# Kernel optimization log

Hardware: AMD Instinct MI355X
Metric: run time of the kernel (lower is better)

## Reference

```python
import jax, jax.numpy as jnp
import numpy as np

B, N, M, D = 8, 4096, 4096, 2


def setup_inputs() -> dict:
    key = jax.random.key(0)
    k1, k2, k3, k4 = jax.random.split(key, 4)
    return {
        "predicted_coords": jax.random.normal(k1, (B, N, D), dtype=jnp.float32),
        "predicted_points": jax.random.randint(k2, (B,), N // 2, N + 1, dtype=jnp.int32),
        "target_coords": jax.random.normal(k3, (B, M, D), dtype=jnp.float32),
        "target_points": jax.random.randint(k4, (B,), M // 2, M + 1, dtype=jnp.int32),
    }


def reference(predicted_coords, predicted_points, target_coords, target_points):
    # predicted_coords: [B, N, D], target_coords: [B, M, D]
    # predicted_points / target_points: [B] valid counts
    n = predicted_coords.shape[1]
    d = predicted_coords.shape[2]

    # points_loss = MSE(pred_counts/N, target_counts/N) over the batch
    points_loss = jnp.mean(
        (predicted_points.astype(jnp.float32) / n - target_points.astype(jnp.float32) / n) ** 2
    )

    # Batched 1-NN: squared pairwise distances [B, N, M], invalid targets masked to +inf.
    # (argmin of squared Euclidean == argmin of Euclidean, matching KDTree k=1.)
    d2 = jnp.sum((predicted_coords[:, :, None, :] - target_coords[:, None, :, :]) ** 2, axis=-1)
    tmask = jnp.arange(target_coords.shape[1])[None, :] < target_points[:, None]  # [B, M]
    d2 = jnp.where(tmask[:, None, :], d2, jnp.inf)
    idx = jnp.argmin(d2, axis=-1)  # [B, N]

    # Matched targets are detached in the original (numpy round-trip) -> stop_gradient.
    matched = jax.lax.stop_gradient(
        jnp.take_along_axis(target_coords, idx[:, :, None], axis=1)
    )  # [B, N, D]

    sq = jnp.sum((predicted_coords - matched) ** 2, axis=-1)  # [B, N]
    pmask = jnp.arange(predicted_coords.shape[1])[None, :] < predicted_points[:, None]  # [B, N]
    # Per-sample MSE over valid pred points (mean over count*D elements), then mean over batch.
    denom = predicted_points.astype(jnp.float32) * d
    coord_loss = jnp.mean(jnp.sum(jnp.where(pmask, sq, 0.0), axis=-1) / denom)

    total_loss = coord_loss + 0.1 * points_loss
    return (total_loss, coord_loss, points_loss)
```

## Files before the change

kernel.cpp:

```cpp
#include <hip/hip_runtime.h>
#include <math.h>

#define NB 8
#define NPTS 4096
#define MPTS 4096
#define CHUNK 64
#define NCHUNK (NPTS / CHUNK)
#define NWAVE 8
#define TQ (MPTS / NWAVE)

__device__ __forceinline__ float waveReduceSum(float v) {
#pragma unroll
    for (int off = 32; off > 0; off >>= 1)
        v += __shfl_down(v, off, 64);
    return v;
}

__global__ __launch_bounds__(NWAVE * 64) void nn_kernel(
    const float2* __restrict__ pred,
    const int* __restrict__ pcounts,
    const float2* __restrict__ tgt,
    const int* __restrict__ tcounts,
    float* __restrict__ partials)
{
    __shared__ float sx[MPTS];
    __shared__ float sy[MPTS];
    __shared__ float sc[MPTS];
    __shared__ float mnw[NWAVE][CHUNK];

    const int g = blockIdx.x;
    const int b = g >> 6;
    const int c = g & (NCHUNK - 1);
    const int w = threadIdx.x >> 6;
    const int lane = threadIdx.x & 63;

    const int tcount = tcounts[b];
    const int tstart = w * TQ;

    const float2* tsrc = tgt + (size_t)b * MPTS + tstart;
#pragma unroll
    for (int i = 0; i < TQ / 64; ++i) {
        float2 t = tsrc[i * 64 + lane];
        int idx = tstart + i * 64 + lane;
        sx[idx] = -2.0f * t.x;
        sy[idx] = -2.0f * t.y;
        sc[idx] = fmaf(t.x, t.x, t.y * t.y);
    }

    const float2 p = pred[(size_t)b * NPTS + c * CHUNK + lane];

    int tloc = min(tcount - tstart, TQ);
    if (tloc < 0) tloc = 0;

    float m0 = INFINITY, m1 = INFINITY, m2 = INFINITY, m3 = INFINITY;
    const float4* x4 = (const float4*)&sx[tstart];
    const float4* y4 = (const float4*)&sy[tstart];
    const float4* c4 = (const float4*)&sc[tstart];
    const int nt4 = tloc >> 2;
    for (int i = 0; i < nt4; ++i) {
        float4 xv = x4[i], yv = y4[i], cv = c4[i];
        m0 = fminf(m0, fmaf(p.y, yv.x, fmaf(p.x, xv.x, cv.x)));
        m1 = fminf(m1, fmaf(p.y, yv.y, fmaf(p.x, xv.y, cv.y)));
        m2 = fminf(m2, fmaf(p.y, yv.z, fmaf(p.x, xv.z, cv.z)));
        m3 = fminf(m3, fmaf(p.y, yv.w, fmaf(p.x, xv.w, cv.w)));
    }
    for (int m = nt4 * 4; m < tloc; ++m) {
        float v = fmaf(p.y, sy[tstart + m], fmaf(p.x, sx[tstart + m], sc[tstart + m]));
        m0 = fminf(m0, v);
    }
    mnw[w][lane] = fminf(fminf(m0, m1), fminf(m2, m3));
    __syncthreads();

    if (w == 0) {
        float mn = mnw[0][lane];
#pragma unroll
        for (int j = 1; j < NWAVE; ++j) mn = fminf(mn, mnw[j][lane]);
        float pp = fmaf(p.x, p.x, p.y * p.y);
        float v = (c * CHUNK + lane < pcounts[b]) ? (mn + pp) : 0.0f;
        v = waveReduceSum(v);
        if (lane == 0) partials[g] = v;
    }
}

__global__ __launch_bounds__(512) void final_kernel(
    const float* __restrict__ partials,
    const int* __restrict__ pcounts,
    const int* __restrict__ tcounts,
    float* __restrict__ out)
{
    __shared__ float bs[NB];
    const int w = threadIdx.x >> 6;
    const int lane = threadIdx.x & 63;
    float v = partials[w * NCHUNK + lane];
    v = waveReduceSum(v);
    if (lane == 0) bs[w] = v;
    __syncthreads();
    if (threadIdx.x == 0) {
        float coord = 0.0f, pts = 0.0f;
        for (int b = 0; b < NB; ++b) {
            coord += bs[b] / ((float)pcounts[b] * 2.0f);
            float d = ((float)pcounts[b] - (float)tcounts[b]) / (float)NPTS;
            pts += d * d;
        }
        coord *= (1.0f / NB);
        pts *= (1.0f / NB);
        out[0] = coord + 0.1f * pts;
        out[1] = coord;
        out[2] = pts;
    }
}

extern "C" void kernel_launch(void* const* d_in, const int* in_sizes, int n_in,
                              void* d_out, int out_size, void* d_ws, size_t ws_size,
                              hipStream_t stream) {
    const float2* pred    = (const float2*)d_in[0];
    const int*    pcounts = (const int*)d_in[1];
    const float2* tgt     = (const float2*)d_in[2];
    const int*    tcounts = (const int*)d_in[3];
    float* out = (float*)d_out;

    float* partials = (float*)d_ws;

    nn_kernel<<<NB * NCHUNK, NWAVE * 64, 0, stream>>>(
        pred, pcounts, tgt, tcounts, partials);
    final_kernel<<<1, 512, 0, stream>>>(partials, pcounts, tcounts, out);
}
```

Measured before the change: 20.33 us.

## Split target set across blocks with register-blocked preds and separate min-combine kernel

Restructures the nearest-neighbor search so each block handles a 128-target slice for 1024 predictions, with each thread keeping 4 predictions in registers to reuse every shared-memory target load. Partial minima per slice go to a workspace buffer of 32 slices. A new combine kernel takes the min across slices, adds the squared norm, masks invalid predictions and reduces. The aim is less shared-memory load traffic per FMA and no full-target staging per block, at the cost of an extra kernel launch and about 4 MB of global writes and reads for the partial minima.

```diff
diff --git a/kernel.cpp b/kernel.cpp
--- a/kernel.cpp
+++ b/kernel.cpp
@@ -4,10 +4,15 @@
 #define NB 8
 #define NPTS 4096
 #define MPTS 4096
-#define CHUNK 64
-#define NCHUNK (NPTS / CHUNK)
-#define NWAVE 8
-#define TQ (MPTS / NWAVE)
+#define BN (NB * NPTS)
+#define P 4
+#define WV 4
+#define TT 128
+#define NS (MPTS / TT)
+#define PREDS_PER_WAVE (64 * P)
+#define PREDS_PER_BLOCK (PREDS_PER_WAVE * WV)
+#define PGROUPS (BN / PREDS_PER_BLOCK)
+#define NCHUNK 64
 
 __device__ __forceinline__ float waveReduceSum(float v) {
 #pragma unroll
@@ -16,70 +21,99 @@
     return v;
 }
 
-__global__ __launch_bounds__(NWAVE * 64) void nn_kernel(
+__global__ __launch_bounds__(WV * 64) void nn_kernel(
+    const float2* __restrict__ pred,
+    const float2* __restrict__ tgt,
+    const int* __restrict__ tcounts,
+    float* __restrict__ mins)
+{
+    __shared__ float sx[TT];
+    __shared__ float sy[TT];
+    __shared__ float sc[TT];
+    const int bid = blockIdx.x;
+    const int s  = bid & (NS - 1);
+    const int pg = bid >> 5;
+    const int b  = pg >> 2;
+    const int tid = threadIdx.x;
+
+    const int tcount = tcounts[b];
+    const int tstart = s * TT;
+    const int tloc = min(tcount - tstart, TT);
+
+    if (tid < TT) {
+        float2 t = tgt[(size_t)b * MPTS + tstart + tid];
+        sx[tid] = -2.0f * t.x;
+        sy[tid] = -2.0f * t.y;
+        sc[tid] = fmaf(t.x, t.x, t.y * t.y);
+    }
+    __syncthreads();
+
+    const int w = tid >> 6, lane = tid & 63;
+    const size_t pbase = (size_t)pg * PREDS_PER_BLOCK + w * PREDS_PER_WAVE + lane;
+    const float2 p0 = pred[pbase];
+    const float2 p1 = pred[pbase + 64];
+    const float2 p2 = pred[pbase + 128];
+    const float2 p3 = pred[pbase + 192];
+
+    float mn0 = INFINITY, mn1 = INFINITY, mn2 = INFINITY, mn3 = INFINITY;
+
+    if (tloc > 0) {
+        const float4* x4 = (const float4*)sx;
+        const float4* y4 = (const float4*)sy;
+        const float4* c4 = (const float4*)sc;
+        const int nt4 = tloc >> 2;
+#pragma unroll 2
+        for (int i = 0; i < nt4; ++i) {
+            float4 xv = x4[i], yv = y4[i], cv = c4[i];
+            mn0 = fminf(mn0, fmaf(p0.y, yv.x, fmaf(p0.x, xv.x, cv.x)));
+            mn1 = fminf(mn1, fmaf(p1.y, yv.x, fmaf(p1.x, xv.x, cv.x)));
+            mn2 = fminf(mn2, fmaf(p2.y, yv.x, fmaf(p2.x, xv.x, cv.x)));
+            mn3 = fminf(mn3, fmaf(p3.y, yv.x, fmaf(p3.x, xv.x, cv.x)));
+            mn0 = fminf(mn0, fmaf(p0.y, yv.y, fmaf(p0.x, xv.y, cv.y)));
+            mn1 = fminf(mn1, fmaf(p1.y, yv.y, fmaf(p1.x, xv.y, cv.y)));
+            mn2 = fminf(mn2, fmaf(p2.y, yv.y, fmaf(p2.x, xv.y, cv.y)));
+            mn3 = fminf(mn3, fmaf(p3.y, yv.y, fmaf(p3.x, xv.y, cv.y)));
+            mn0 = fminf(mn0, fmaf(p0.y, yv.z, fmaf(p0.x, xv.z, cv.z)));
+            mn1 = fminf(mn1, fmaf(p1.y, yv.z, fmaf(p1.x, xv.z, cv.z)));
+            mn2 = fminf(mn2, fmaf(p2.y, yv.z, fmaf(p2.x, xv.z, cv.z)));
+            mn3 = fminf(mn3, fmaf(p3.y, yv.z, fmaf(p3.x, xv.z, cv.z)));
+            mn0 = fminf(mn0, fmaf(p0.y, yv.w, fmaf(p0.x, xv.w, cv.w)));
+            mn1 = fminf(mn1, fmaf(p1.y, yv.w, fmaf(p1.x, xv.w, cv.w)));
+            mn2 = fminf(mn2, fmaf(p2.y, yv.w, fmaf(p2.x, xv.w, cv.w)));
+            mn3 = fminf(mn3, fmaf(p3.y, yv.w, fmaf(p3.x, xv.w, cv.w)));
+        }
+        for (int m = nt4 * 4; m < tloc; ++m) {
+            float xs = sx[m], ys = sy[m], cs = sc[m];
+            mn0 = fminf(mn0, fmaf(p0.y, ys, fmaf(p0.x, xs, cs)));
+            mn1 = fminf(mn1, fmaf(p1.y, ys, fmaf(p1.x, xs, cs)));
+            mn2 = fminf(mn2, fmaf(p2.y, ys, fmaf(p2.x, xs, cs)));
+            mn3 = fminf(mn3, fmaf(p3.y, ys, fmaf(p3.x, xs, cs)));
+        }
+    }
+    float* dst = mins + (size_t)s * BN + pbase;
+    dst[0]   = mn0;
+    dst[64]  = mn1;
+    dst[128] = mn2;
+    dst[192] = mn3;
+}
+
+__global__ __launch_bounds__(256) void combine_kernel(
+    const float* __restrict__ mins,
     const float2* __restrict__ pred,
     const int* __restrict__ pcounts,
-    const float2* __restrict__ tgt,
-    const int* __restrict__ tcounts,
     float* __restrict__ partials)
 {
-    __shared__ float sx[MPTS];
-    __shared__ float sy[MPTS];
-    __shared__ float sc[MPTS];
-    __shared__ float mnw[NWAVE][CHUNK];
-
-    const int g = blockIdx.x;
-    const int b = g >> 6;
-    const int c = g & (NCHUNK - 1);
-    const int w = threadIdx.x >> 6;
-    const int lane = threadIdx.x & 63;
-
-    const int tcount = tcounts[b];
-    const int tstart = w * TQ;
-
-    const float2* tsrc = tgt + (size_t)b * MPTS + tstart;
+    const int idx = blockIdx.x * 256 + threadIdx.x;
+    const int b = idx >> 12;
+    const int n = idx & (NPTS - 1);
+    float v = mins[idx];
 #pragma unroll
-    for (int i = 0; i < TQ / 64; ++i) {
-        float2 t = tsrc[i * 64 + lane];
-        int idx = tstart + i * 64 + lane;
-        sx[idx] = -2.0f * t.x;
-        sy[idx] = -2.0f * t.y;
-        sc[idx] = fmaf(t.x, t.x, t.y * t.y);
-    }
-
-    const float2 p = pred[(size_t)b * NPTS + c * CHUNK + lane];
-
-    int tloc = min(tcount - tstart, TQ);
-    if (tloc < 0) tloc = 0;
-
-    float m0 = INFINITY, m1 = INFINITY, m2 = INFINITY, m3 = INFINITY;
-    const float4* x4 = (const float4*)&sx[tstart];
-    const float4* y4 = (const float4*)&sy[tstart];
-    const float4* c4 = (const float4*)&sc[tstart];
-    const int nt4 = tloc >> 2;
-    for (int i = 0; i < nt4; ++i) {
-        float4 xv = x4[i], yv = y4[i], cv = c4[i];
-        m0 = fminf(m0, fmaf(p.y, yv.x, fmaf(p.x, xv.x, cv.x)));
-        m1 = fminf(m1, fmaf(p.y, yv.y, fmaf(p.x, xv.y, cv.y)));
-        m2 = fminf(m2, fmaf(p.y, yv.z, fmaf(p.x, xv.z, cv.z)));
-        m3 = fminf(m3, fmaf(p.y, yv.w, fmaf(p.x, xv.w, cv.w)));
-    }
-    for (int m = nt4 * 4; m < tloc; ++m) {
-        float v = fmaf(p.y, sy[tstart + m], fmaf(p.x, sx[tstart + m], sc[tstart + m]));
-        m0 = fminf(m0, v);
-    }
-    mnw[w][lane] = fminf(fminf(m0, m1), fminf(m2, m3));
-    __syncthreads();
-
-    if (w == 0) {
-        float mn = mnw[0][lane];
-#pragma unroll
-        for (int j = 1; j < NWAVE; ++j) mn = fminf(mn, mnw[j][lane]);
-        float pp = fmaf(p.x, p.x, p.y * p.y);
-        float v = (c * CHUNK + lane < pcounts[b]) ? (mn + pp) : 0.0f;
-        v = waveReduceSum(v);
-        if (lane == 0) partials[g] = v;
-    }
+    for (int s = 1; s < NS; ++s) v = fminf(v, mins[(size_t)s * BN + idx]);
+    float2 p = pred[idx];
+    v += fmaf(p.x, p.x, p.y * p.y);
+    v = (n < pcounts[b]) ? v : 0.0f;
+    v = waveReduceSum(v);
+    if ((threadIdx.x & 63) == 0) partials[idx >> 6] = v;
 }
 
 __global__ __launch_bounds__(512) void final_kernel(
@@ -120,8 +154,9 @@
     float* out = (float*)d_out;
 
     float* partials = (float*)d_ws;
+    float* mins     = partials + NB * NCHUNK;
 
-    nn_kernel<<<NB * NCHUNK, NWAVE * 64, 0, stream>>>(
-        pred, pcounts, tgt, tcounts, partials);
+    nn_kernel<<<PGROUPS * NS, WV * 64, 0, stream>>>(pred, tgt, tcounts, mins);
+    combine_kernel<<<BN / 256, 256, 0, stream>>>(mins, pred, pcounts, partials);
     final_kernel<<<1, 512, 0, stream>>>(partials, pcounts, tcounts, out);
 }
```

New measurement: 19.69 us. -3.1%, faster.
